# Performance work log

Hardware: AMD Instinct MI355X
Metric: run time of the kernel (lower is better)

## Reference

```python
import jax, jax.numpy as jnp
import numpy as np

B, T, C, H = 4, 2048, 768, 12
D = C // H  # head dim = 64
EPS = 1e-5


def setup_inputs() -> dict:
    key = jax.random.key(0)
    ks = jax.random.split(key, 12)
    s = lambda fan_in: 1.0 / np.sqrt(fan_in)
    return {
        "x": jax.random.normal(ks[0], (B, T, C), dtype=jnp.float32),
        "ln1_g": jnp.ones((C,), jnp.float32),
        "ln1_b": jnp.zeros((C,), jnp.float32),
        "w_attn": jax.random.normal(ks[1], (C, 3 * C), jnp.float32) * s(C),
        "b_attn": jnp.zeros((3 * C,), jnp.float32),
        "w_aproj": jax.random.normal(ks[2], (C, C), jnp.float32) * s(C),
        "b_aproj": jnp.zeros((C,), jnp.float32),
        "ln2_g": jnp.ones((C,), jnp.float32),
        "ln2_b": jnp.zeros((C,), jnp.float32),
        "w_fc": jax.random.normal(ks[3], (C, 4 * C), jnp.float32) * s(C),
        "b_fc": jnp.zeros((4 * C,), jnp.float32),
        "w_mproj": jax.random.normal(ks[4], (4 * C, C), jnp.float32) * s(4 * C),
        "b_mproj": jnp.zeros((C,), jnp.float32),
    }


def _layernorm(x, g, b):
    mu = jnp.mean(x, axis=-1, keepdims=True)
    var = jnp.mean(jnp.square(x - mu), axis=-1, keepdims=True)
    return (x - mu) * jax.lax.rsqrt(var + EPS) * g + b


def _attention(h, w_attn, b_attn, w_aproj, b_aproj):
    qkv = h @ w_attn + b_attn                          # [B,T,3C]
    q, k, v = jnp.split(qkv, 3, axis=-1)
    q = q.reshape(B, T, H, D)
    k = k.reshape(B, T, H, D)
    v = v.reshape(B, T, H, D)
    att = jnp.einsum("bqhd,bkhd->bhqk", q, k) * (1.0 / np.sqrt(D))
    causal = jnp.tril(jnp.ones((T, T), bool))
    att = jnp.where(causal, att, -jnp.inf)
    att = jax.nn.softmax(att, axis=-1)
    y = jnp.einsum("bhqk,bkhd->bqhd", att, v).reshape(B, T, C)
    return y @ w_aproj + b_aproj


def reference(x, ln1_g, ln1_b, w_attn, b_attn, w_aproj, b_aproj,
              ln2_g, ln2_b, w_fc, b_fc, w_mproj, b_mproj):
    x = x + _attention(_layernorm(x, ln1_g, ln1_b), w_attn, b_attn, w_aproj, b_aproj)
    h = _layernorm(x, ln2_g, ln2_b)
    h = jax.nn.gelu(h @ w_fc + b_fc, approximate=True)  # tanh approximation, matches F.gelu(approximate='tanh')
    x = x + (h @ w_mproj + b_mproj)
    return x
```

## Files before the change

### kernel.cpp

```cpp
#include <hip/hip_runtime.h>


typedef unsigned short ushortT;
typedef unsigned int uintT;
typedef __attribute__((ext_vector_type(8))) __bf16 bf16x8;
typedef __attribute__((ext_vector_type(4))) float f32x4;

#define MFMA16(a, b, c) __builtin_amdgcn_mfma_f32_16x16x32_bf16(a, b, c, 0, 0, 0)

__device__ inline float b2f(ushortT u) {
  return __uint_as_float(((uintT)u) << 16);
}
__device__ inline ushortT f2b(float f) {
  uintT x = __float_as_uint(f);
  uintT r = x + 0x7fffu + ((x >> 16) & 1u);
  return (ushortT)(r >> 16);
}
__device__ inline uintT pack_bf2(float a, float b) {
  return __builtin_amdgcn_perm(__float_as_uint(b), __float_as_uint(a),
                               0x07060302u);
}

__device__ inline float fast_exp2(float x) {
#if __has_builtin(__builtin_amdgcn_exp2f)
  return __builtin_amdgcn_exp2f(x);
#else
  return exp2f(x);
#endif
}

__device__ inline float gelu_tanh(float v) {
  float t = 0.7978845608028654f * (v + 0.044715f * v * v * v);
  return v / (1.0f + __expf(-2.0f * t));
}

__device__ __forceinline__ void glds16(const ushortT* g, ushortT* l) {
  __builtin_amdgcn_global_load_lds(
      (const __attribute__((address_space(1))) unsigned int*)(const void*)g,
      (__attribute__((address_space(3))) unsigned int*)(void*)l, 16, 0, 0);
}

struct VecArgs {
  const void* src[8];
  int n[8];
  int dstoff[8];
};

__global__ __launch_bounds__(256) void prep_kernel(
    const void* __restrict__ w_attn, const void* __restrict__ w_aproj,
    const void* __restrict__ w_fc, const void* __restrict__ w_mproj,
    VecArgs va, ushortT* __restrict__ wT0, ushortT* __restrict__ wT1,
    ushortT* __restrict__ wT2, ushortT* __restrict__ wT3,
    ushortT* __restrict__ pv, int* __restrict__ flag) {
  __shared__ int sfl;
  __shared__ ushortT tile[32][33];
  int tid = threadIdx.x;
  {
    int crazy = 0;
    if (tid < 64) {
      uintT e = (((const ushortT*)w_fc)[2 * (tid * 64)] >> 7) & 0xFF;
      crazy = (e >= 150) ? 1 : 0;
    }
    unsigned long long m = __ballot(crazy != 0);
    if (tid == 0) sfl = (m != 0ull) ? 1 : 0;
    __syncthreads();
  }
  int fl = sfl;
  int b = (int)blockIdx.x;
  if (b == 0 && tid == 0) *flag = fl;

  const int T0 = 1728;
  const int T1 = T0 + 576;
  const int T2 = T1 + 2304;
  const int T3 = T2 + 2304;

  const void* in = nullptr;
  ushortT* out = nullptr;
  int K = 0, N = 0, gx = 0, t = 0;
  if (b < T0)      { in = w_attn;  out = wT0; K = 768;  N = 2304; gx = 72; t = b; }
  else if (b < T1) { in = w_aproj; out = wT1; K = 768;  N = 768;  gx = 24; t = b - T0; }
  else if (b < T2) { in = w_fc;    out = wT2; K = 768;  N = 3072; gx = 96; t = b - T1; }
  else if (b < T3) { in = w_mproj; out = wT3; K = 3072; N = 768;  gx = 24; t = b - T2; }
  else {
    int c = b - T3;
    int v = 0;
    for (;;) {
      int nch = (va.n[v] + 255) >> 8;
      if (c < nch) break;
      c -= nch; ++v;
    }
    int i = c * 256 + tid;
    if (i < va.n[v]) {
      float x = fl ? ((const float*)va.src[v])[i]
                   : b2f(((const ushortT*)va.src[v])[i]);
      pv[va.dstoff[v] + i] = f2b(x);
    }
    return;
  }

  int n0 = (t % gx) * 32, k0 = (t / gx) * 32;
  int x = tid & 31, y0 = tid >> 5;
#pragma unroll
  for (int i = y0; i < 32; i += 8) {
    size_t idx = (size_t)(k0 + i) * N + n0 + x;
    tile[i][x] = fl ? f2b(((const float*)in)[idx]) : ((const ushortT*)in)[idx];
  }
  __syncthreads();
#pragma unroll
  for (int i = y0; i < 32; i += 8)
    out[(size_t)(n0 + i) * K + k0 + x] = tile[x][i];
}

__global__ __launch_bounds__(256) void vtrans_kernel(
    const ushortT* __restrict__ qkv, ushortT* __restrict__ vt) {
  const int T = 2048, C3 = 2304;
  __shared__ ushortT tile[64][65];
  int bh = blockIdx.y;
  int b = bh / 12, h = bh % 12;
  int t0 = blockIdx.x * 64;
  int col = threadIdx.x & 63, rowi = threadIdx.x >> 6;
#pragma unroll
  for (int rr = rowi; rr < 64; rr += 4)
    tile[rr][col] =
        qkv[((size_t)(b * T + t0 + rr)) * C3 + 1536 + h * 64 + col];
  __syncthreads();
#pragma unroll
  for (int dd = rowi; dd < 64; dd += 4)
    vt[((size_t)bh * 64 + dd) * T + t0 + col] = tile[col][dd];
}

template <int MODE>
__global__ __launch_bounds__(256) void ln_kernel(
    const void* __restrict__ xin, const ushortT* __restrict__ g,
    const ushortT* __restrict__ bb, ushortT* __restrict__ out,
    const int* __restrict__ flag) {
  const int C = 768;
  bool f32;
  if constexpr (MODE == 1) f32 = true; else f32 = (*flag != 0);
  size_t base = (size_t)blockIdx.x * C;
  int tid = threadIdx.x;
  const float* xf = (const float*)xin;
  const ushortT* xb = (const ushortT*)xin;
  float v0 = f32 ? xf[base + tid]       : b2f(xb[base + tid]);
  float v1 = f32 ? xf[base + tid + 256] : b2f(xb[base + tid + 256]);
  float v2 = f32 ? xf[base + tid + 512] : b2f(xb[base + tid + 512]);
  float s = v0 + v1 + v2;
  float q = v0 * v0 + v1 * v1 + v2 * v2;
#pragma unroll
  for (int off = 32; off; off >>= 1) {
    s += __shfl_xor(s, off);
    q += __shfl_xor(q, off);
  }
  __shared__ float as_[4], aq_[4];
  if ((tid & 63) == 0) { as_[tid >> 6] = s; aq_[tid >> 6] = q; }
  __syncthreads();
  s = as_[0] + as_[1] + as_[2] + as_[3];
  q = aq_[0] + aq_[1] + aq_[2] + aq_[3];
  float mu = s * (1.0f / 768.0f);
  float var = q * (1.0f / 768.0f) - mu * mu;
  float rs = rsqrtf(var + 1e-5f);
  ushortT* orow = out + base;
  orow[tid]       = f2b((v0 - mu) * rs * b2f(g[tid])       + b2f(bb[tid]));
  orow[tid + 256] = f2b((v1 - mu) * rs * b2f(g[tid + 256]) + b2f(bb[tid + 256]));
  orow[tid + 512] = f2b((v2 - mu) * rs * b2f(g[tid + 512]) + b2f(bb[tid + 512]));
}

template <int EPI, int BN>
__global__ __launch_bounds__(256, 2) void gemm_8p(
    const ushortT* __restrict__ A, const ushortT* __restrict__ Bt,
    const ushortT* __restrict__ bias, const void* __restrict__ res,
    void* __restrict__ out, int N, int K, int lda, int nbm, int nbn,
    const int* __restrict__ flag) {
  constexpr int MI = (BN == 256) ? 8 : 4;
  constexpr int NI = 4;
  __shared__ ushortT As3[3][128 * 32];
  __shared__ ushortT Bs3[3][BN * 32];
  int fl = (EPI >= 2) ? *flag : 0;
  int tid = threadIdx.x;
  int lane = tid & 63, wave = tid >> 6;
  int quad = lane >> 4, n = lane & 15;
  int wm, wn;
  if constexpr (BN == 256) { wm = 0; wn = wave * 64; }
  else { wm = (wave >> 1) * 64; wn = (wave & 1) * 64; }
  int l = blockIdx.x;
  int xcd = l & 7, j = l >> 3;
  int per = (nbm >> 3) * nbn;
  int js = j % per, sp = j / per;
  int m0 = (xcd * (nbm >> 3) + js / nbn) * 128;
  int n0 = (js % nbn) * BN;
  int koff = sp * K;

  int trow = tid >> 2;
  int tc = (((tid & 3) ^ ((trow >> 1) & 3)) << 3);
  const ushortT* ga = A + (size_t)(m0 + trow) * lda + koff + tc;
  const ushortT* gb = Bt + (size_t)(n0 + trow) * lda + koff + tc;

  const int cs = (quad ^ ((n >> 1) & 3)) << 3;

  int kt = K >> 5;
  f32x4 acc[MI][NI] = {};

  auto stage = [&](int tt, int slot) {
    int k0 = tt << 5;
    ushortT* la = &As3[slot][0] + wave * 512;
    ushortT* lb = &Bs3[slot][0] + wave * 512;
    glds16(ga + k0, la);
    glds16(ga + (size_t)64 * lda + k0, la + 2048);
    glds16(gb + k0, lb);
    glds16(gb + (size_t)64 * lda + k0, lb + 2048);
    if constexpr (BN == 256) {
      glds16(gb + (size_t)128 * lda + k0, lb + 4096);
      glds16(gb + (size_t)192 * lda + k0, lb + 6144);
    }
  };

  stage(0, 0);
  stage(1, 1);
  if constexpr (BN == 256)
    asm volatile("s_waitcnt vmcnt(6)" ::: "memory");
  else
    asm volatile("s_waitcnt vmcnt(4)" ::: "memory");
  __builtin_amdgcn_s_barrier();

  int cur = 0;
  for (int t = 0; t < kt; ++t) {
    const ushortT* ca = &As3[cur][0];
    const ushortT* cb = &Bs3[cur][0];
    int nxt = cur + 2; if (nxt >= 3) nxt -= 3;
    bool pf = (t + 2) < kt;
    int pk0 = (t + 2) << 5;
    ushortT* la = &As3[nxt][0] + wave * 512;
    ushortT* lb = &Bs3[nxt][0] + wave * 512;

    bf16x8 af[4], bfr[NI];
#pragma unroll
    for (int i = 0; i < 4; ++i)
      af[i] = *(const bf16x8*)(ca + (wm + i * 16 + n) * 32 + cs);
#pragma unroll
    for (int i = 0; i < NI; ++i)
      bfr[i] = *(const bf16x8*)(cb + (wn + i * 16 + n) * 32 + cs);
    if (pf) {
      glds16(ga + pk0, la);
      glds16(ga + (size_t)64 * lda + pk0, la + 2048);
      glds16(gb + pk0, lb);
      if constexpr (BN == 128)
        glds16(gb + (size_t)64 * lda + pk0, lb + 2048);
    }
    __builtin_amdgcn_s_barrier();
    __builtin_amdgcn_s_setprio(1);
#pragma unroll
    for (int mi = 0; mi < 4; ++mi)
#pragma unroll
      for (int ni = 0; ni < NI; ++ni)
        acc[mi][ni] = MFMA16(af[mi], bfr[ni], acc[mi][ni]);
    __builtin_amdgcn_s_setprio(0);
    if constexpr (BN == 256) {
      __builtin_amdgcn_s_barrier();
#pragma unroll
      for (int i = 0; i < 4; ++i)
        af[i] = *(const bf16x8*)(ca + (64 + i * 16 + n) * 32 + cs);
      if (pf) {
        glds16(gb + (size_t)64 * lda + pk0, lb + 2048);
        glds16(gb + (size_t)128 * lda + pk0, lb + 4096);
        glds16(gb + (size_t)192 * lda + pk0, lb + 6144);
      }
      __builtin_amdgcn_s_barrier();
      __builtin_amdgcn_s_setprio(1);
#pragma unroll
      for (int mi = 0; mi < 4; ++mi)
#pragma unroll
        for (int ni = 0; ni < NI; ++ni)
          acc[4 + mi][ni] = MFMA16(af[mi], bfr[ni], acc[4 + mi][ni]);
      __builtin_amdgcn_s_setprio(0);
    }
    if (pf) {
      if constexpr (BN == 256)
        asm volatile("s_waitcnt vmcnt(6)" ::: "memory");
      else
        asm volatile("s_waitcnt vmcnt(4)" ::: "memory");
    } else {
      asm volatile("s_waitcnt vmcnt(0)" ::: "memory");
    }
    __builtin_amdgcn_s_barrier();

    cur = cur + 1; if (cur == 3) cur = 0;
  }

  float* po = nullptr;
  if constexpr (EPI == 4) po = sp ? (float*)res : (float*)out;
#pragma unroll
  for (int mi = 0; mi < MI; ++mi) {
#pragma unroll
    for (int ni = 0; ni < NI; ++ni) {
      int gc = n0 + wn + ni * 16 + n;
      float bv = (EPI == 4) ? 0.0f : b2f(bias[gc]);
      int gr0 = m0 + wm + mi * 16 + quad * 4;
#pragma unroll
      for (int r = 0; r < 4; ++r) {
        size_t idx = (size_t)(gr0 + r) * N + gc;
        float v = acc[mi][ni][r] + bv;
        if constexpr (EPI == 1) {
          v = gelu_tanh(v);
          ((ushortT*)out)[idx] = f2b(v);
        } else if constexpr (EPI == 2) {
          v += fl ? ((const float*)res)[idx] : b2f(((const ushortT*)res)[idx]);
          ((float*)out)[idx] = v;
        } else if constexpr (EPI == 3) {
          v += ((const float*)res)[idx];
          if (fl) ((float*)out)[idx] = v;
          else    ((ushortT*)out)[idx] = f2b(v);
        } else if constexpr (EPI == 4) {
          po[idx] = v;
        } else {
          ((ushortT*)out)[idx] = f2b(v);
        }
      }
    }
  }
}

__global__ __launch_bounds__(256) void attn_kernel(
    const ushortT* __restrict__ qkv, const ushortT* __restrict__ vt,
    ushortT* __restrict__ y) {
  const int T = 2048, C3 = 2304;
  constexpr int LDP = 72;
  __shared__ ushortT Ks[2][64 * 64];
  __shared__ ushortT Vs[2][64 * 64];
  __shared__ ushortT Ps[4 * 16 * LDP];
  int bh = blockIdx.y;
  int b = bh / 12, h = bh % 12;
  int pj = blockIdx.x;
  int tid = threadIdx.x;
  int lane = tid & 63, wave = tid >> 6;
  int quad = lane >> 4, n = lane & 15, n7 = n & 7;

  const ushortT* base = qkv + (size_t)b * T * C3;
  const ushortT* kbase = base + 768 + h * 64;
  const ushortT* vbase = vt + (size_t)bh * 64 * T;
  ushortT* myP = Ps + wave * 16 * LDP;

  const float QS = 0.18033688011112042f;
  const float MB = 20.0f;

  int qtA = pj, qtB = 31 - pj;
  int nA = qtA + 1, ntot = 33;

  int srow = lane >> 3, scol = lane & 7;
  const ushortT* kg =
      kbase + (size_t)(wave * 16 + srow) * C3 + ((scol ^ srow) << 3);
  const ushortT* vg =
      vbase + (size_t)(wave * 16 + srow) * T + ((scol ^ srow) << 3);

  const int c0 = (quad ^ n7) << 3;
  const int c1 = ((4 + quad) ^ n7) << 3;

  int qt = qtA;
  int qw = qt * 64 + wave * 16;
  bf16x8 aq[2];
  {
    const ushortT* qrow = base + (size_t)(qw + n) * C3 + h * 64 + quad * 8;
#pragma unroll
    for (int dh = 0; dh < 2; ++dh) {
      union { ushortT u[8]; bf16x8 v; } tmp;
#pragma unroll
      for (int j = 0; j < 8; ++j) tmp.u[j] = f2b(b2f(qrow[dh * 32 + j]) * QS);
      aq[dh] = tmp.v;
    }
  }
  f32x4 Ot[4] = {};
  float l_ = 0.f;

  auto stage = [&](int kt_, int buf) {
    int kof = kt_ << 6;
    ushortT* lk = &Ks[buf][0] + wave * 1024;
    ushortT* lv = &Vs[buf][0] + wave * 1024;
    glds16(kg + (size_t)kof * C3, lk);
    glds16(kg + (size_t)(kof + 8) * C3, lk + 512);
    glds16(vg + kof, lv);
    glds16(vg + (size_t)8 * T + kof, lv + 512);
  };

  stage(0, 0);
  __syncthreads();

  int cur = 0;
  for (int t = 0; t < ntot; ++t) {
    int kt = (t < nA) ? t : t - nA;
    if (t + 1 < ntot) {
      int ktn = (t + 1 < nA) ? t + 1 : t + 1 - nA;
      stage(ktn, cur ^ 1);
    }
    const ushortT* ks = &Ks[cur][0];
    const ushortT* vs = &Vs[cur][0];

    f32x4 St[4];
#pragma unroll
    for (int g = 0; g < 4; ++g) {
      bf16x8 ka0 = *(const bf16x8*)(ks + (g * 16 + n) * 64 + c0);
      bf16x8 ka1 = *(const bf16x8*)(ks + (g * 16 + n) * 64 + c1);
      f32x4 z = {};
      z = MFMA16(ka0, aq[0], z);
      St[g] = MFMA16(ka1, aq[1], z);
    }
    if (kt == qt) {
      int lim = wave * 16 + n;
#pragma unroll
      for (int g = 0; g < 4; ++g)
#pragma unroll
        for (int r = 0; r < 4; ++r)
          if (g * 16 + quad * 4 + r > lim) St[g][r] = -1e30f;
    }
    float ls = 0.f;
#pragma unroll
    for (int g = 0; g < 4; ++g) {
      float p0 = fast_exp2(St[g][0] - MB);
      float p1 = fast_exp2(St[g][1] - MB);
      float p2 = fast_exp2(St[g][2] - MB);
      float p3 = fast_exp2(St[g][3] - MB);
      ls += (p0 + p1) + (p2 + p3);
      uint2 pk;
      pk.x = pack_bf2(p0, p1);
      pk.y = pack_bf2(p2, p3);
      *(uint2*)(myP + n * LDP + g * 16 + quad * 4) = pk;
    }
    ls += __shfl_xor(ls, 16);
    ls += __shfl_xor(ls, 32);
    l_ += ls;

    bf16x8 pb0 = *(const bf16x8*)(myP + n * LDP + quad * 8);
    bf16x8 pb1 = *(const bf16x8*)(myP + n * LDP + 32 + quad * 8);
#pragma unroll
    for (int dt = 0; dt < 4; ++dt) {
      bf16x8 va0 = *(const bf16x8*)(vs + (dt * 16 + n) * 64 + c0);
      bf16x8 va1 = *(const bf16x8*)(vs + (dt * 16 + n) * 64 + c1);
      Ot[dt] = MFMA16(va0, pb0, Ot[dt]);
      Ot[dt] = MFMA16(va1, pb1, Ot[dt]);
    }

    if (kt == qt) {
      float inv = 1.0f / l_;
      int qg = qw + n;
#pragma unroll
      for (int dt = 0; dt < 4; ++dt) {
        uint2 o;
        o.x = pack_bf2(Ot[dt][0] * inv, Ot[dt][1] * inv);
        o.y = pack_bf2(Ot[dt][2] * inv, Ot[dt][3] * inv);
        *(uint2*)(y + (size_t)(b * T + qg) * 768 + h * 64 + dt * 16 +
                  quad * 4) = o;
      }
      if (t + 1 < ntot) {
        qt = qtB;
        qw = qt * 64 + wave * 16;
        const ushortT* qrow =
            base + (size_t)(qw + n) * C3 + h * 64 + quad * 8;
#pragma unroll
        for (int dh = 0; dh < 2; ++dh) {
          union { ushortT u[8]; bf16x8 v; } tmp;
#pragma unroll
          for (int j = 0; j < 8; ++j)
            tmp.u[j] = f2b(b2f(qrow[dh * 32 + j]) * QS);
          aq[dh] = tmp.v;
        }
#pragma unroll
        for (int dt = 0; dt < 4; ++dt)
#pragma unroll
          for (int r = 0; r < 4; ++r) Ot[dt][r] = 0.f;
        l_ = 0.f;
      }
    }
    __syncthreads();
    cur ^= 1;
  }
}

extern "C" void kernel_launch(void* const* d_in, const int* in_sizes, int n_in,
                              void* d_out, int out_size, void* d_ws,
                              size_t ws_size, hipStream_t stream) {
  (void)in_sizes; (void)n_in; (void)out_size; (void)ws_size;
  const void* x       = d_in[0];
  const void* w_attn  = d_in[3];
  const void* w_aproj = d_in[5];
  const void* w_fc    = d_in[9];
  const void* w_mproj = d_in[11];

  char* ws = (char*)d_ws;
  ushortT* h1  = (ushortT*)(ws);
  ushortT* qkv = (ushortT*)(ws + 12582912);
  ushortT* yb  = (ushortT*)(ws + 50331648);
  float*   x1  = (float*)(ws + 62914560);
  ushortT* fcg = (ushortT*)(ws + 88080384);
  ushortT* wT0 = (ushortT*)(ws + 138412032);
  ushortT* wT1 = (ushortT*)(ws + 141950976);
  ushortT* wT2 = (ushortT*)(ws + 143130624);
  ushortT* wT3 = (ushortT*)(ws + 147849216);
  ushortT* pv  = (ushortT*)(ws + 152567808);
  int*     flag = (int*)(ws + 152600576);
  ushortT* vt  = h1;
  ushortT* h2  = yb;

  const int O_LN1G = 0, O_LN1B = 768, O_BATT = 1536, O_BAPR = 3840,
            O_LN2G = 4608, O_LN2B = 5376, O_BFC = 6144, O_BMPR = 9216;

  VecArgs va;
  va.src[0] = d_in[1];  va.n[0] = 768;  va.dstoff[0] = O_LN1G;
  va.src[1] = d_in[2];  va.n[1] = 768;  va.dstoff[1] = O_LN1B;
  va.src[2] = d_in[4];  va.n[2] = 2304; va.dstoff[2] = O_BATT;
  va.src[3] = d_in[6];  va.n[3] = 768;  va.dstoff[3] = O_BAPR;
  va.src[4] = d_in[7];  va.n[4] = 768;  va.dstoff[4] = O_LN2G;
  va.src[5] = d_in[8];  va.n[5] = 768;  va.dstoff[5] = O_LN2B;
  va.src[6] = d_in[10]; va.n[6] = 3072; va.dstoff[6] = O_BFC;
  va.src[7] = d_in[12]; va.n[7] = 768;  va.dstoff[7] = O_BMPR;

  prep_kernel<<<6951, 256, 0, stream>>>(
      w_attn, w_aproj, w_fc, w_mproj, va, wT0, wT1, wT2, wT3, pv, flag);

  ln_kernel<0><<<8192, 256, 0, stream>>>(x, pv + O_LN1G, pv + O_LN1B, h1, flag);
  gemm_8p<0, 256><<<576, 256, 0, stream>>>(
      h1, wT0, pv + O_BATT, nullptr, qkv, 2304, 768, 768, 64, 9, flag);
  vtrans_kernel<<<dim3(32, 48), 256, 0, stream>>>(qkv, vt);
  attn_kernel<<<dim3(16, 48), 256, 0, stream>>>(qkv, vt, yb);
  gemm_8p<2, 128><<<384, 256, 0, stream>>>(
      yb, wT1, pv + O_BAPR, x, x1, 768, 768, 768, 64, 6, flag);
  ln_kernel<1><<<8192, 256, 0, stream>>>(x1, pv + O_LN2G, pv + O_LN2B, h2, flag);
  gemm_8p<1, 256><<<768, 256, 0, stream>>>(
      h2, wT2, pv + O_BFC, nullptr, fcg, 3072, 768, 768, 64, 12, flag);
  gemm_8p<3, 128><<<384, 256, 0, stream>>>(
      fcg, wT3, pv + O_BMPR, x1, d_out, 768, 3072, 3072, 64, 6, flag);
}
```

Before: 409.1 us.

## Fuse LN1 into prep kernel and V-transpose into QKV GEMM epilogue

Folds the first layernorm into the weight-prep launch as extra blocks, and has the QKV GEMM epilogue write V directly in transposed per-head layout, which removes the separate vtrans kernel. It also drops the unused split-K path from the GEMM. This cuts two kernel launches and one full read and write of V. In exchange, the transposed V store is a strided 8-byte write, and the V buffer now aliases fcg.

Result: no change. 402.0 us (-1.7%).

```diff
diff --git a/kernel.cpp b/kernel.cpp
--- a/kernel.cpp
+++ b/kernel.cpp
@@ -51,9 +51,12 @@
     const void* __restrict__ w_fc, const void* __restrict__ w_mproj,
     VecArgs va, ushortT* __restrict__ wT0, ushortT* __restrict__ wT1,
     ushortT* __restrict__ wT2, ushortT* __restrict__ wT3,
-    ushortT* __restrict__ pv, int* __restrict__ flag) {
+    ushortT* __restrict__ pv, int* __restrict__ flag,
+    const void* __restrict__ x, const void* __restrict__ ln1g,
+    const void* __restrict__ ln1b, ushortT* __restrict__ h1) {
   __shared__ int sfl;
   __shared__ ushortT tile[32][33];
+  __shared__ float as_[4], aq_[4];
   int tid = threadIdx.x;
   {
     int crazy = 0;
@@ -73,6 +76,45 @@
   const int T1 = T0 + 576;
   const int T2 = T1 + 2304;
   const int T3 = T2 + 2304;
+  const int T4 = T3 + 39;
+
+  if (b >= T4) {
+    int row = b - T4;
+    size_t base = (size_t)row * 768;
+    const float* xf = (const float*)x;
+    const ushortT* xb = (const ushortT*)x;
+    float v0 = fl ? xf[base + tid]       : b2f(xb[base + tid]);
+    float v1 = fl ? xf[base + tid + 256] : b2f(xb[base + tid + 256]);
+    float v2 = fl ? xf[base + tid + 512] : b2f(xb[base + tid + 512]);
+    float s = v0 + v1 + v2;
+    float q = v0 * v0 + v1 * v1 + v2 * v2;
+#pragma unroll
+    for (int off = 32; off; off >>= 1) {
+      s += __shfl_xor(s, off);
+      q += __shfl_xor(q, off);
+    }
+    if ((tid & 63) == 0) { as_[tid >> 6] = s; aq_[tid >> 6] = q; }
+    __syncthreads();
+    s = as_[0] + as_[1] + as_[2] + as_[3];
+    q = aq_[0] + aq_[1] + aq_[2] + aq_[3];
+    float mu = s * (1.0f / 768.0f);
+    float var = q * (1.0f / 768.0f) - mu * mu;
+    float rs = rsqrtf(var + 1e-5f);
+    const float* gf = (const float*)ln1g;
+    const ushortT* gb_ = (const ushortT*)ln1g;
+    const float* bf = (const float*)ln1b;
+    const ushortT* bb_ = (const ushortT*)ln1b;
+    ushortT* orow = h1 + base;
+#pragma unroll
+    for (int jj = 0; jj < 3; ++jj) {
+      int c = tid + jj * 256;
+      float gv = fl ? gf[c] : b2f(gb_[c]);
+      float bv = fl ? bf[c] : b2f(bb_[c]);
+      float vv = (jj == 0) ? v0 : (jj == 1) ? v1 : v2;
+      orow[c] = f2b((vv - mu) * rs * gv + bv);
+    }
+    return;
+  }
 
   const void* in = nullptr;
   ushortT* out = nullptr;
@@ -91,42 +133,24 @@
     }
     int i = c * 256 + tid;
     if (i < va.n[v]) {
-      float x = fl ? ((const float*)va.src[v])[i]
-                   : b2f(((const ushortT*)va.src[v])[i]);
-      pv[va.dstoff[v] + i] = f2b(x);
+      float xx = fl ? ((const float*)va.src[v])[i]
+                    : b2f(((const ushortT*)va.src[v])[i]);
+      pv[va.dstoff[v] + i] = f2b(xx);
     }
     return;
   }
 
   int n0 = (t % gx) * 32, k0 = (t / gx) * 32;
-  int x = tid & 31, y0 = tid >> 5;
+  int xx = tid & 31, y0 = tid >> 5;
 #pragma unroll
   for (int i = y0; i < 32; i += 8) {
-    size_t idx = (size_t)(k0 + i) * N + n0 + x;
-    tile[i][x] = fl ? f2b(((const float*)in)[idx]) : ((const ushortT*)in)[idx];
+    size_t idx = (size_t)(k0 + i) * N + n0 + xx;
+    tile[i][xx] = fl ? f2b(((const float*)in)[idx]) : ((const ushortT*)in)[idx];
   }
   __syncthreads();
 #pragma unroll
   for (int i = y0; i < 32; i += 8)
-    out[(size_t)(n0 + i) * K + k0 + x] = tile[x][i];
-}
-
-__global__ __launch_bounds__(256) void vtrans_kernel(
-    const ushortT* __restrict__ qkv, ushortT* __restrict__ vt) {
-  const int T = 2048, C3 = 2304;
-  __shared__ ushortT tile[64][65];
-  int bh = blockIdx.y;
-  int b = bh / 12, h = bh % 12;
-  int t0 = blockIdx.x * 64;
-  int col = threadIdx.x & 63, rowi = threadIdx.x >> 6;
-#pragma unroll
-  for (int rr = rowi; rr < 64; rr += 4)
-    tile[rr][col] =
-        qkv[((size_t)(b * T + t0 + rr)) * C3 + 1536 + h * 64 + col];
-  __syncthreads();
-#pragma unroll
-  for (int dd = rowi; dd < 64; dd += 4)
-    vt[((size_t)bh * 64 + dd) * T + t0 + col] = tile[col][dd];
+    out[(size_t)(n0 + i) * K + k0 + xx] = tile[xx][i];
 }
 
 template <int MODE>
@@ -175,7 +199,7 @@
   constexpr int NI = 4;
   __shared__ ushortT As3[3][128 * 32];
   __shared__ ushortT Bs3[3][BN * 32];
-  int fl = (EPI >= 2) ? *flag : 0;
+  int fl = (EPI == 2 || EPI == 3) ? *flag : 0;
   int tid = threadIdx.x;
   int lane = tid & 63, wave = tid >> 6;
   int quad = lane >> 4, n = lane & 15;
@@ -184,16 +208,13 @@
   else { wm = (wave >> 1) * 64; wn = (wave & 1) * 64; }
   int l = blockIdx.x;
   int xcd = l & 7, j = l >> 3;
-  int per = (nbm >> 3) * nbn;
-  int js = j % per, sp = j / per;
-  int m0 = (xcd * (nbm >> 3) + js / nbn) * 128;
-  int n0 = (js % nbn) * BN;
-  int koff = sp * K;
+  int m0 = (xcd * (nbm >> 3) + j / nbn) * 128;
+  int n0 = (j % nbn) * BN;
 
   int trow = tid >> 2;
   int tc = (((tid & 3) ^ ((trow >> 1) & 3)) << 3);
-  const ushortT* ga = A + (size_t)(m0 + trow) * lda + koff + tc;
-  const ushortT* gb = Bt + (size_t)(n0 + trow) * lda + koff + tc;
+  const ushortT* ga = A + (size_t)(m0 + trow) * lda + tc;
+  const ushortT* gb = Bt + (size_t)(n0 + trow) * lda + tc;
 
   const int cs = (quad ^ ((n >> 1) & 3)) << 3;
 
@@ -286,33 +307,51 @@
     cur = cur + 1; if (cur == 3) cur = 0;
   }
 
-  float* po = nullptr;
-  if constexpr (EPI == 4) po = sp ? (float*)res : (float*)out;
 #pragma unroll
   for (int mi = 0; mi < MI; ++mi) {
 #pragma unroll
     for (int ni = 0; ni < NI; ++ni) {
       int gc = n0 + wn + ni * 16 + n;
-      float bv = (EPI == 4) ? 0.0f : b2f(bias[gc]);
+      float bv = b2f(bias[gc]);
       int gr0 = m0 + wm + mi * 16 + quad * 4;
-#pragma unroll
-      for (int r = 0; r < 4; ++r) {
-        size_t idx = (size_t)(gr0 + r) * N + gc;
-        float v = acc[mi][ni][r] + bv;
-        if constexpr (EPI == 1) {
-          v = gelu_tanh(v);
-          ((ushortT*)out)[idx] = f2b(v);
-        } else if constexpr (EPI == 2) {
-          v += fl ? ((const float*)res)[idx] : b2f(((const ushortT*)res)[idx]);
-          ((float*)out)[idx] = v;
-        } else if constexpr (EPI == 3) {
-          v += ((const float*)res)[idx];
-          if (fl) ((float*)out)[idx] = v;
-          else    ((ushortT*)out)[idx] = f2b(v);
-        } else if constexpr (EPI == 4) {
-          po[idx] = v;
+      if constexpr (EPI == 5) {
+        float v0 = acc[mi][ni][0] + bv;
+        float v1 = acc[mi][ni][1] + bv;
+        float v2 = acc[mi][ni][2] + bv;
+        float v3 = acc[mi][ni][3] + bv;
+        if (gc < 1536) {
+          ushortT* o = (ushortT*)out;
+          o[(size_t)(gr0 + 0) * N + gc] = f2b(v0);
+          o[(size_t)(gr0 + 1) * N + gc] = f2b(v1);
+          o[(size_t)(gr0 + 2) * N + gc] = f2b(v2);
+          o[(size_t)(gr0 + 3) * N + gc] = f2b(v3);
         } else {
-          ((ushortT*)out)[idx] = f2b(v);
+          int hh = (gc - 1536) >> 6, dd = (gc - 1536) & 63;
+          int bb = gr0 >> 11, tin = gr0 & 2047;
+          ushortT* vp = (ushortT*)res;
+          uint2 o;
+          o.x = (uintT)f2b(v0) | ((uintT)f2b(v1) << 16);
+          o.y = (uintT)f2b(v2) | ((uintT)f2b(v3) << 16);
+          *(uint2*)(vp + ((size_t)(bb * 12 + hh) * 64 + dd) * 2048 + tin) = o;
+        }
+      } else {
+#pragma unroll
+        for (int r = 0; r < 4; ++r) {
+          size_t idx = (size_t)(gr0 + r) * N + gc;
+          float v = acc[mi][ni][r] + bv;
+          if constexpr (EPI == 1) {
+            v = gelu_tanh(v);
+            ((ushortT*)out)[idx] = f2b(v);
+          } else if constexpr (EPI == 2) {
+            v += fl ? ((const float*)res)[idx] : b2f(((const ushortT*)res)[idx]);
+            ((float*)out)[idx] = v;
+          } else if constexpr (EPI == 3) {
+            v += ((const float*)res)[idx];
+            if (fl) ((float*)out)[idx] = v;
+            else    ((ushortT*)out)[idx] = f2b(v);
+          } else {
+            ((ushortT*)out)[idx] = f2b(v);
+          }
         }
       }
     }
@@ -495,7 +534,7 @@
   ushortT* wT3 = (ushortT*)(ws + 147849216);
   ushortT* pv  = (ushortT*)(ws + 152567808);
   int*     flag = (int*)(ws + 152600576);
-  ushortT* vt  = h1;
+  ushortT* vt  = fcg;
   ushortT* h2  = yb;
 
   const int O_LN1G = 0, O_LN1B = 768, O_BATT = 1536, O_BAPR = 3840,
@@ -511,13 +550,12 @@
   va.src[6] = d_in[10]; va.n[6] = 3072; va.dstoff[6] = O_BFC;
   va.src[7] = d_in[12]; va.n[7] = 768;  va.dstoff[7] = O_BMPR;
 
-  prep_kernel<<<6951, 256, 0, stream>>>(
-      w_attn, w_aproj, w_fc, w_mproj, va, wT0, wT1, wT2, wT3, pv, flag);
-
-  ln_kernel<0><<<8192, 256, 0, stream>>>(x, pv + O_LN1G, pv + O_LN1B, h1, flag);
-  gemm_8p<0, 256><<<576, 256, 0, stream>>>(
-      h1, wT0, pv + O_BATT, nullptr, qkv, 2304, 768, 768, 64, 9, flag);
-  vtrans_kernel<<<dim3(32, 48), 256, 0, stream>>>(qkv, vt);
+  prep_kernel<<<15143, 256, 0, stream>>>(
+      w_attn, w_aproj, w_fc, w_mproj, va, wT0, wT1, wT2, wT3, pv, flag,
+      x, d_in[1], d_in[2], h1);
+
+  gemm_8p<5, 256><<<576, 256, 0, stream>>>(
+      h1, wT0, pv + O_BATT, vt, qkv, 2304, 768, 768, 64, 9, flag);
   attn_kernel<<<dim3(16, 48), 256, 0, stream>>>(qkv, vt, yb);
   gemm_8p<2, 128><<<384, 256, 0, stream>>>(
       yb, wT1, pv + O_BAPR, x, x1, 768, 768, 768, 64, 6, flag);
```
